# Kernel optimization log

Hardware: AMD Instinct MI355X
Metric: run time of the kernel (lower is better)

## Reference

```python
import jax, jax.numpy as jnp
import numpy as np

N_NODES = 100000
N_EDGES = 1600000
D_IN = 128
D_HID = 128
N_CLASSES = 8


def setup_inputs() -> dict:
    key = jax.random.key(0)
    ks = jax.random.split(key, 8)
    x = jax.random.normal(ks[0], (N_NODES, D_IN), dtype=jnp.float32)
    edge_index = jax.random.randint(ks[1], (2, N_EDGES), 0, N_NODES, dtype=jnp.int32)
    # Glorot-ish init for weights, zeros for biases (PyG GCNConv default)
    W1 = jax.random.normal(ks[2], (D_IN, D_HID), dtype=jnp.float32) / np.sqrt(D_IN)
    b1 = jnp.zeros((D_HID,), dtype=jnp.float32)
    W2 = jax.random.normal(ks[3], (D_HID, D_HID), dtype=jnp.float32) / np.sqrt(D_HID)
    b2 = jnp.zeros((D_HID,), dtype=jnp.float32)
    Wout = jax.random.normal(ks[4], (D_HID, N_CLASSES), dtype=jnp.float32) / np.sqrt(D_HID)
    bout = jnp.zeros((N_CLASSES,), dtype=jnp.float32)
    return {"x": x, "edge_index": edge_index, "W1": W1, "b1": b1,
            "W2": W2, "b2": b2, "Wout": Wout, "bout": bout}


def _gcn_conv(h, src, dst, norm, W, b, n_nodes):
    # h: [N, d_in]; src/dst: [E+N] (with self-loops); norm: [E+N]
    h = h @ W                                   # [N, d_out]
    msg = h[src] * norm[:, None]                # gather + edge-wise scale
    agg = jax.ops.segment_sum(msg, dst, num_segments=n_nodes)  # scatter-add
    return agg + b


def reference(x, edge_index, W1, b1, W2, b2, Wout, bout):
    n = x.shape[0]
    loops = jnp.arange(n, dtype=edge_index.dtype)
    src = jnp.concatenate([edge_index[0], loops])   # [E+N]
    dst = jnp.concatenate([edge_index[1], loops])   # [E+N]
    # symmetric normalization D^-1/2 (A+I) D^-1/2
    deg = jax.ops.segment_sum(jnp.ones_like(src, dtype=x.dtype), dst, num_segments=n)
    dinv = jnp.where(deg > 0, jax.lax.rsqrt(deg), 0.0)
    norm = dinv[src] * dinv[dst]                    # [E+N]

    h = _gcn_conv(x, src, dst, norm, W1, b1, n)
    h = jax.nn.relu(h)  # dropout is identity in eval mode
    h = _gcn_conv(h, src, dst, norm, W2, b2, n)
    h = jax.nn.relu(h)
    return jax.nn.softmax(h @ Wout + bout, axis=1)  # [N, 8]
```

## Files before the change

### kernel.cpp

```cpp
#include <hip/hip_runtime.h>
#include <hip/hip_fp16.h>

#define NN 100000
#define NE 1600000
#define D 128
#define NC 8
#define NBUCK 391
#define BCAP 6144
#define CHUNK 4096
#define NBLK_SC ((NE + CHUNK - 1) / CHUNK)

typedef _Float16 half8 __attribute__((ext_vector_type(8)));
typedef float f32x4 __attribute__((ext_vector_type(4)));

__global__ __launch_bounds__(256) void k_scat(const int* __restrict__ src,
                                              const int* __restrict__ dst,
                                              int* __restrict__ bcursor,
                                              int* __restrict__ staged,
                                              const float* __restrict__ W1,
                                              __half* __restrict__ wt1,
                                              const float* __restrict__ W2,
                                              __half* __restrict__ wt2, int E) {
    const int t = threadIdx.x;
    if (blockIdx.x >= NBLK_SC) {
        const float* W = (blockIdx.x - NBLK_SC) ? W2 : W1;
        __half* wt = (blockIdx.x - NBLK_SC) ? wt2 : wt1;
        for (int i = t; i < D * D; i += 256) {
            int k = i >> 7, c = i & 127;
            wt[c * D + k] = __float2half(W[i]);
        }
        return;
    }
    __shared__ int h[NBUCK];
    __shared__ int cur[NBUCK];
    for (int i = t; i < NBUCK; i += 256) h[i] = 0;
    __syncthreads();
    const int base0 = blockIdx.x * CHUNK;
    int4 d4[4], s4[4];
    bool val[4];
#pragma unroll
    for (int i = 0; i < 4; ++i) {
        int e = base0 + i * 1024 + t * 4;
        val[i] = e < E;
        if (val[i]) {
            d4[i] = *(const int4*)&dst[e];
            s4[i] = *(const int4*)&src[e];
            atomicAdd(&h[d4[i].x >> 8], 1);
            atomicAdd(&h[d4[i].y >> 8], 1);
            atomicAdd(&h[d4[i].z >> 8], 1);
            atomicAdd(&h[d4[i].w >> 8], 1);
        }
    }
    __syncthreads();
    for (int i = t; i < NBUCK; i += 256) {
        int c = h[i];
        cur[i] = c ? (i * BCAP + atomicAdd(&bcursor[i], c)) : 0;
    }
    __syncthreads();
#pragma unroll
    for (int i = 0; i < 4; ++i) {
        if (val[i]) {
            int p;
            p = atomicAdd(&cur[d4[i].x >> 8], 1); staged[p] = s4[i].x * 256 + (d4[i].x & 255);
            p = atomicAdd(&cur[d4[i].y >> 8], 1); staged[p] = s4[i].y * 256 + (d4[i].y & 255);
            p = atomicAdd(&cur[d4[i].z >> 8], 1); staged[p] = s4[i].z * 256 + (d4[i].z & 255);
            p = atomicAdd(&cur[d4[i].w >> 8], 1); staged[p] = s4[i].w * 256 + (d4[i].w & 255);
        }
    }
}

template <bool F32IN, bool SCALE>
__device__ __forceinline__ void gemm_body(const void* __restrict__ Ain,
                                          const __half* __restrict__ wt,
                                          const float* __restrict__ dinv,
                                          __half* __restrict__ hout, int gb) {
    const int tid = threadIdx.x;
    const int lane = tid & 63;
    const int wave = tid >> 6;
    const int wr = wave >> 1, wc = wave & 1;
    const int row0 = gb * 32 + wr * 16;
    const int arow = row0 + (lane & 15);
    const int kg = lane >> 4;

    half8 afrag[4];
    if constexpr (F32IN) {
        const float* A = (const float*)Ain;
#pragma unroll
        for (int s = 0; s < 4; ++s) {
            const float* p = &A[(size_t)arow * D + s * 32 + kg * 8];
            float4 f0 = *(const float4*)p;
            float4 f1 = *(const float4*)(p + 4);
            half8 a;
            a[0] = (_Float16)f0.x; a[1] = (_Float16)f0.y;
            a[2] = (_Float16)f0.z; a[3] = (_Float16)f0.w;
            a[4] = (_Float16)f1.x; a[5] = (_Float16)f1.y;
            a[6] = (_Float16)f1.z; a[7] = (_Float16)f1.w;
            afrag[s] = a;
        }
    } else {
        const __half* A = (const __half*)Ain;
#pragma unroll
        for (int s = 0; s < 4; ++s)
            afrag[s] = *(const half8*)&A[(size_t)arow * D + s * 32 + kg * 8];
    }

    f32x4 acc[4] = {};
    const int colbase = wc * 64;
#pragma unroll
    for (int c = 0; c < 4; ++c) {
        const int col = colbase + c * 16 + (lane & 15);
#pragma unroll
        for (int s = 0; s < 4; ++s) {
            half8 b = *(const half8*)&wt[col * D + s * 32 + kg * 8];
            acc[c] = __builtin_amdgcn_mfma_f32_16x16x32_f16(afrag[s], b, acc[c], 0, 0, 0);
        }
    }

#pragma unroll
    for (int r = 0; r < 4; ++r) {
        const int row = row0 + kg * 4 + r;
        float dv = 1.0f;
        if constexpr (SCALE) dv = dinv[row];
#pragma unroll
        for (int c = 0; c < 4; ++c) {
            const int col = colbase + c * 16 + (lane & 15);
            hout[(size_t)row * D + col] = __float2half(SCALE ? acc[c][r] * dv : acc[c][r]);
        }
    }
}

__global__ __launch_bounds__(256) void k_fg(const int* __restrict__ staged,
                                            const int* __restrict__ bcursor,
                                            int* __restrict__ rowstart,
                                            int* __restrict__ cnt,
                                            float* __restrict__ dinv,
                                            int* __restrict__ csr,
                                            const float* __restrict__ x,
                                            const __half* __restrict__ wt1,
                                            __half* __restrict__ hout) {
    const int b = blockIdx.x;
    if (b >= NBUCK) {
        gemm_body<true, false>(x, wt1, nullptr, hout, b - NBUCK);
        return;
    }
    const int t = threadIdx.x;
    const int bs = b * BCAP;
    const int be = bs + bcursor[b];
    __shared__ int lc[256];
    __shared__ int ls[256];
    __shared__ int sd[256];
    lc[t] = 0;
    __syncthreads();
    for (int i = bs + t; i < be; i += 256) {
        atomicAdd(&lc[staged[i] & 255], 1);
    }
    __syncthreads();
    int v = lc[t];
    sd[t] = v;
    __syncthreads();
    for (int off = 1; off < 256; off <<= 1) {
        int y = (t >= off) ? sd[t - off] : 0;
        __syncthreads();
        sd[t] += y;
        __syncthreads();
    }
    int ex = sd[t] - v;
    ls[t] = bs + ex;
    int node = (b << 8) + t;
    if (node < NN) {
        rowstart[node] = bs + ex;
        cnt[node] = v;
        dinv[node] = rsqrtf((float)(v + 1));
    }
    lc[t] = 0;
    __syncthreads();
    for (int i = bs + t; i < be; i += 256) {
        int e = staged[i];
        int li = e & 255;
        int p = atomicAdd(&lc[li], 1);
        csr[ls[li] + p] = e >> 8;
    }
}

__global__ __launch_bounds__(256) void k_gemm2(const __half* __restrict__ A,
                                               const __half* __restrict__ wt,
                                               const float* __restrict__ dinv,
                                               __half* __restrict__ hout) {
    gemm_body<false, true>(A, wt, dinv, hout, blockIdx.x);
}

__device__ inline void add8h(float* acc, float4 raw) {
    const __half2* hp = (const __half2*)&raw;
#pragma unroll
    for (int q = 0; q < 4; ++q) {
        float2 f = __half22float2(hp[q]);
        acc[2 * q] += f.x;
        acc[2 * q + 1] += f.y;
    }
}

__device__ inline void fma8h(float* acc, float4 raw, float s) {
    const __half2* hp = (const __half2*)&raw;
#pragma unroll
    for (int q = 0; q < 4; ++q) {
        float2 f = __half22float2(hp[q]);
        acc[2 * q] = fmaf(s, f.x, acc[2 * q]);
        acc[2 * q + 1] = fmaf(s, f.y, acc[2 * q + 1]);
    }
}

__global__ __launch_bounds__(256) void k_agg_u(const __half* __restrict__ hs,
                                               const int* __restrict__ rowstart,
                                               const int* __restrict__ cnt,
                                               const int* __restrict__ csr_src,
                                               const float* __restrict__ dinv,
                                               const float* __restrict__ bias,
                                               __half* __restrict__ hout) {
    const int node = blockIdx.x * 4 + (threadIdx.x >> 6);
    const int lane = threadIdx.x & 63;
    const int g = lane >> 4;
    const int f8 = (lane & 15) << 3;

    const float dvn = dinv[node];
    float acc[8] = {};
    if (g == 0) fma8h(acc, *(const float4*)&hs[(size_t)node * D + f8], dvn);

    const int c = cnt[node];
    const int* __restrict__ cl = csr_src + rowstart[node];

    int t = g;
    while (t < c) {
        float4 v[8];
        float dv8[8];
#pragma unroll
        for (int i = 0; i < 8; ++i) {
            int tt = t + 4 * i;
            if (tt < c) {
                int s = cl[tt];
                v[i] = *(const float4*)&hs[(size_t)s * D + f8];
                dv8[i] = dinv[s];
            }
        }
#pragma unroll
        for (int i = 0; i < 8; ++i) {
            int tt = t + 4 * i;
            if (tt < c) fma8h(acc, v[i], dv8[i]);
        }
        t += 32;
    }

#pragma unroll
    for (int q = 0; q < 8; ++q) {
        acc[q] += __shfl_xor(acc[q], 16);
        acc[q] += __shfl_xor(acc[q], 32);
    }

    if (g == 0) {
        float r[8];
#pragma unroll
        for (int q = 0; q < 8; ++q) r[q] = fmaxf(fmaf(dvn, acc[q], bias[f8 + q]), 0.f);
        union { float4 f; __half2 h[4]; } u;
#pragma unroll
        for (int q = 0; q < 4; ++q) u.h[q] = __floats2half2_rn(r[2 * q], r[2 * q + 1]);
        *(float4*)&hout[(size_t)node * D + f8] = u.f;
    }
}

__global__ __launch_bounds__(256) void k_agg_s(const __half* __restrict__ hs,
                                               const int* __restrict__ rowstart,
                                               const int* __restrict__ cnt,
                                               const int* __restrict__ csr_src,
                                               const float* __restrict__ dinv,
                                               const float* __restrict__ bias,
                                               __half* __restrict__ hout) {
    const int node = blockIdx.x * 4 + (threadIdx.x >> 6);
    const int lane = threadIdx.x & 63;
    const int g = lane >> 4;
    const int f8 = (lane & 15) << 3;

    float acc[8] = {};
    if (g == 0) add8h(acc, *(const float4*)&hs[(size_t)node * D + f8]);

    const int c = cnt[node];
    const int* __restrict__ cl = csr_src + rowstart[node];

    int t = g;
    while (t < c) {
        float4 v[8];
#pragma unroll
        for (int i = 0; i < 8; ++i) {
            int tt = t + 4 * i;
            if (tt < c) {
                int s = cl[tt];
                v[i] = *(const float4*)&hs[(size_t)s * D + f8];
            }
        }
#pragma unroll
        for (int i = 0; i < 8; ++i) {
            int tt = t + 4 * i;
            if (tt < c) add8h(acc, v[i]);
        }
        t += 32;
    }

#pragma unroll
    for (int q = 0; q < 8; ++q) {
        acc[q] += __shfl_xor(acc[q], 16);
        acc[q] += __shfl_xor(acc[q], 32);
    }

    if (g == 0) {
        const float dv = dinv[node];
        float r[8];
#pragma unroll
        for (int q = 0; q < 8; ++q) r[q] = fmaxf(fmaf(dv, acc[q], bias[f8 + q]), 0.f);
        union { float4 f; __half2 h[4]; } u;
#pragma unroll
        for (int q = 0; q < 4; ++q) u.h[q] = __floats2half2_rn(r[2 * q], r[2 * q + 1]);
        *(float4*)&hout[(size_t)node * D + f8] = u.f;
    }
}

__global__ void k_out(const __half* __restrict__ h, const float* __restrict__ Wout,
                      const float* __restrict__ bout, float* __restrict__ out, int n) {
    __shared__ float ws[D * NC];
    int tid = threadIdx.x;
    for (int i = tid; i < D * NC; i += 256) ws[i] = Wout[i];
    __syncthreads();
    int node = blockIdx.x * 32 + (tid >> 3);
    int c = tid & 7;
    if (node >= n) return;
    float acc = bout[c];
    const __half* hrow = &h[(size_t)node * D];
#pragma unroll
    for (int k8 = 0; k8 < 16; ++k8) {
        float4 raw = *(const float4*)&hrow[k8 * 8];
        const __half2* hp = (const __half2*)&raw;
#pragma unroll
        for (int q = 0; q < 4; ++q) {
            float2 f = __half22float2(hp[q]);
            int k = k8 * 8 + 2 * q;
            acc += f.x * ws[k * NC + c] + f.y * ws[(k + 1) * NC + c];
        }
    }
    float m = acc;
#pragma unroll
    for (int off = 1; off < 8; off <<= 1) m = fmaxf(m, __shfl_xor(m, off));
    float e = __expf(acc - m);
    float ssum = e;
#pragma unroll
    for (int off = 1; off < 8; off <<= 1) ssum += __shfl_xor(ssum, off);
    out[(size_t)node * NC + c] = e / ssum;
}

extern "C" void kernel_launch(void* const* d_in, const int* in_sizes, int n_in,
                              void* d_out, int out_size, void* d_ws, size_t ws_size,
                              hipStream_t stream) {
    const float* x    = (const float*)d_in[0];
    const int*   ei   = (const int*)d_in[1];
    const float* W1   = (const float*)d_in[2];
    const float* b1   = (const float*)d_in[3];
    const float* W2   = (const float*)d_in[4];
    const float* b2   = (const float*)d_in[5];
    const float* Wout = (const float*)d_in[6];
    const float* bout = (const float*)d_in[7];
    float* out = (float*)d_out;

    size_t off = 0;
    char* base = (char*)d_ws;
    auto alloc = [&](size_t bytes) -> void* {
        void* p = base + off;
        off += (bytes + 255) & ~(size_t)255;
        return p;
    };
    int*    cnt      = (int*)alloc((size_t)NN * 4);
    int*    rowstart = (int*)alloc((size_t)NN * 4);
    int*    bcursor  = (int*)alloc((size_t)NBUCK * 4);
    int*    csr      = (int*)alloc((size_t)NBUCK * BCAP * 4);
    float*  dinv     = (float*)alloc((size_t)NN * 4);
    __half* wt1      = (__half*)alloc((size_t)D * D * 2);
    __half* wt2      = (__half*)alloc((size_t)D * D * 2);
    __half* h16a     = (__half*)alloc((size_t)NN * D * 2);
    __half* h16f     = (__half*)alloc((size_t)NN * D * 2);
    __half* h16b     = (__half*)alloc((size_t)NN * D * 2);
    int*    staged   = (int*)alloc((size_t)NBUCK * BCAP * 4);
    if (off > ws_size) return;

    const int* src = ei;
    const int* dst = ei + NE;

    hipMemsetAsync(bcursor, 0, (size_t)NBUCK * 4, stream);

    k_scat<<<NBLK_SC + 2, 256, 0, stream>>>(src, dst, bcursor, staged,
                                            W1, wt1, W2, wt2, NE);

    k_fg<<<NBUCK + NN / 32, 256, 0, stream>>>(staged, bcursor, rowstart, cnt, dinv,
                                              csr, x, wt1, h16a);

    int agg_grid = NN / 4;
    k_agg_u<<<agg_grid, 256, 0, stream>>>(h16a, rowstart, cnt, csr, dinv, b1, h16f);
    k_gemm2<<<NN / 32, 256, 0, stream>>>(h16f, wt2, dinv, h16a);
    k_agg_s<<<agg_grid, 256, 0, stream>>>(h16a, rowstart, cnt, csr, dinv, b2, h16b);
    k_out<<<(NN + 31) / 32, 256, 0, stream>>>(h16b, Wout, bout, out, NN);
}
```

Measured before the change: 269.9 us.

## Fuse layer-1 aggregation with layer-2 GEMM and prescale GEMM1 output by dinv

Splits the old fused CSR-fill plus GEMM1 kernel into a separate bucket-fill kernel followed by GEMM1. GEMM1 now needs dinv, so it prescales rows by dinv and the layer-1 aggregation no longer has to load dinv[src] per edge. The layer-1 aggregation is fused with the layer-2 GEMM: each block aggregates 16 nodes into shared memory and multiplies them by W2 with MFMA. This removes one kernel and one full fp16 intermediate write and read. In exchange, GEMM1 can no longer overlap with the CSR build, and the fused kernel has a barrier and fewer waves per node.

```diff
diff --git a/kernel.cpp b/kernel.cpp
--- a/kernel.cpp
+++ b/kernel.cpp
@@ -69,80 +69,13 @@
     }
 }
 
-template <bool F32IN, bool SCALE>
-__device__ __forceinline__ void gemm_body(const void* __restrict__ Ain,
-                                          const __half* __restrict__ wt,
-                                          const float* __restrict__ dinv,
-                                          __half* __restrict__ hout, int gb) {
-    const int tid = threadIdx.x;
-    const int lane = tid & 63;
-    const int wave = tid >> 6;
-    const int wr = wave >> 1, wc = wave & 1;
-    const int row0 = gb * 32 + wr * 16;
-    const int arow = row0 + (lane & 15);
-    const int kg = lane >> 4;
-
-    half8 afrag[4];
-    if constexpr (F32IN) {
-        const float* A = (const float*)Ain;
-#pragma unroll
-        for (int s = 0; s < 4; ++s) {
-            const float* p = &A[(size_t)arow * D + s * 32 + kg * 8];
-            float4 f0 = *(const float4*)p;
-            float4 f1 = *(const float4*)(p + 4);
-            half8 a;
-            a[0] = (_Float16)f0.x; a[1] = (_Float16)f0.y;
-            a[2] = (_Float16)f0.z; a[3] = (_Float16)f0.w;
-            a[4] = (_Float16)f1.x; a[5] = (_Float16)f1.y;
-            a[6] = (_Float16)f1.z; a[7] = (_Float16)f1.w;
-            afrag[s] = a;
-        }
-    } else {
-        const __half* A = (const __half*)Ain;
-#pragma unroll
-        for (int s = 0; s < 4; ++s)
-            afrag[s] = *(const half8*)&A[(size_t)arow * D + s * 32 + kg * 8];
-    }
-
-    f32x4 acc[4] = {};
-    const int colbase = wc * 64;
-#pragma unroll
-    for (int c = 0; c < 4; ++c) {
-        const int col = colbase + c * 16 + (lane & 15);
-#pragma unroll
-        for (int s = 0; s < 4; ++s) {
-            half8 b = *(const half8*)&wt[col * D + s * 32 + kg * 8];
-            acc[c] = __builtin_amdgcn_mfma_f32_16x16x32_f16(afrag[s], b, acc[c], 0, 0, 0);
-        }
-    }
-
-#pragma unroll
-    for (int r = 0; r < 4; ++r) {
-        const int row = row0 + kg * 4 + r;
-        float dv = 1.0f;
-        if constexpr (SCALE) dv = dinv[row];
-#pragma unroll
-        for (int c = 0; c < 4; ++c) {
-            const int col = colbase + c * 16 + (lane & 15);
-            hout[(size_t)row * D + col] = __float2half(SCALE ? acc[c][r] * dv : acc[c][r]);
-        }
-    }
-}
-
-__global__ __launch_bounds__(256) void k_fg(const int* __restrict__ staged,
-                                            const int* __restrict__ bcursor,
-                                            int* __restrict__ rowstart,
-                                            int* __restrict__ cnt,
-                                            float* __restrict__ dinv,
-                                            int* __restrict__ csr,
-                                            const float* __restrict__ x,
-                                            const __half* __restrict__ wt1,
-                                            __half* __restrict__ hout) {
+__global__ __launch_bounds__(256) void k_bfill(const int* __restrict__ staged,
+                                               const int* __restrict__ bcursor,
+                                               int* __restrict__ rowstart,
+                                               int* __restrict__ cnt,
+                                               float* __restrict__ dinv,
+                                               int* __restrict__ csr) {
     const int b = blockIdx.x;
-    if (b >= NBUCK) {
-        gemm_body<true, false>(x, wt1, nullptr, hout, b - NBUCK);
-        return;
-    }
     const int t = threadIdx.x;
     const int bs = b * BCAP;
     const int be = bs + bcursor[b];
@@ -182,11 +115,54 @@
     }
 }
 
-__global__ __launch_bounds__(256) void k_gemm2(const __half* __restrict__ A,
+__global__ __launch_bounds__(256) void k_gemm1(const float* __restrict__ A,
                                                const __half* __restrict__ wt,
                                                const float* __restrict__ dinv,
                                                __half* __restrict__ hout) {
-    gemm_body<false, true>(A, wt, dinv, hout, blockIdx.x);
+    const int tid = threadIdx.x;
+    const int lane = tid & 63;
+    const int wave = tid >> 6;
+    const int wr = wave >> 1, wc = wave & 1;
+    const int row0 = blockIdx.x * 32 + wr * 16;
+    const int arow = row0 + (lane & 15);
+    const int kg = lane >> 4;
+
+    half8 afrag[4];
+#pragma unroll
+    for (int s = 0; s < 4; ++s) {
+        const float* p = &A[(size_t)arow * D + s * 32 + kg * 8];
+        float4 f0 = *(const float4*)p;
+        float4 f1 = *(const float4*)(p + 4);
+        half8 a;
+        a[0] = (_Float16)f0.x; a[1] = (_Float16)f0.y;
+        a[2] = (_Float16)f0.z; a[3] = (_Float16)f0.w;
+        a[4] = (_Float16)f1.x; a[5] = (_Float16)f1.y;
+        a[6] = (_Float16)f1.z; a[7] = (_Float16)f1.w;
+        afrag[s] = a;
+    }
+
+    f32x4 acc[4] = {};
+    const int colbase = wc * 64;
+#pragma unroll
+    for (int c = 0; c < 4; ++c) {
+        const int col = colbase + c * 16 + (lane & 15);
+#pragma unroll
+        for (int s = 0; s < 4; ++s) {
+            half8 b = *(const half8*)&wt[col * D + s * 32 + kg * 8];
+            acc[c] = __builtin_amdgcn_mfma_f32_16x16x32_f16(afrag[s], b, acc[c], 0, 0, 0);
+        }
+    }
+
+#pragma unroll
+    for (int r = 0; r < 4; ++r) {
+        const int row = row0 + kg * 4 + r;
+        const float dv = dinv[row];
+#pragma unroll
+        for (int c = 0; c < 4; ++c) {
+            const int col = colbase + c * 16 + (lane & 15);
+            hout[(size_t)row * D + col] = __float2half(acc[c][r] * dv);
+        }
+    }
 }
 
 __device__ inline void add8h(float* acc, float4 raw) {
@@ -199,80 +175,96 @@
     }
 }
 
-__device__ inline void fma8h(float* acc, float4 raw, float s) {
-    const __half2* hp = (const __half2*)&raw;
-#pragma unroll
-    for (int q = 0; q < 4; ++q) {
-        float2 f = __half22float2(hp[q]);
-        acc[2 * q] = fmaf(s, f.x, acc[2 * q]);
-        acc[2 * q + 1] = fmaf(s, f.y, acc[2 * q + 1]);
-    }
-}
-
-__global__ __launch_bounds__(256) void k_agg_u(const __half* __restrict__ hs,
-                                               const int* __restrict__ rowstart,
-                                               const int* __restrict__ cnt,
-                                               const int* __restrict__ csr_src,
-                                               const float* __restrict__ dinv,
-                                               const float* __restrict__ bias,
-                                               __half* __restrict__ hout) {
-    const int node = blockIdx.x * 4 + (threadIdx.x >> 6);
+__global__ __launch_bounds__(256) void k_aggemm(const __half* __restrict__ hs,
+                                                const int* __restrict__ rowstart,
+                                                const int* __restrict__ cnt,
+                                                const int* __restrict__ csr_src,
+                                                const float* __restrict__ dinv,
+                                                const float* __restrict__ b1,
+                                                const __half* __restrict__ wt2,
+                                                __half* __restrict__ hout) {
+    __shared__ __align__(16) __half rows[16][136];
+    const int w = threadIdx.x >> 6;
     const int lane = threadIdx.x & 63;
     const int g = lane >> 4;
     const int f8 = (lane & 15) << 3;
-
-    const float dvn = dinv[node];
-    float acc[8] = {};
-    if (g == 0) fma8h(acc, *(const float4*)&hs[(size_t)node * D + f8], dvn);
-
-    const int c = cnt[node];
-    const int* __restrict__ cl = csr_src + rowstart[node];
-
-    int t = g;
-    while (t < c) {
-        float4 v[8];
-        float dv8[8];
-#pragma unroll
-        for (int i = 0; i < 8; ++i) {
-            int tt = t + 4 * i;
-            if (tt < c) {
-                int s = cl[tt];
-                v[i] = *(const float4*)&hs[(size_t)s * D + f8];
-                dv8[i] = dinv[s];
+    const int nb = blockIdx.x * 16;
+
+    for (int k = 0; k < 4; ++k) {
+        const int node = nb + w * 4 + k;
+        float acc[8] = {};
+        if (g == 0) add8h(acc, *(const float4*)&hs[(size_t)node * D + f8]);
+        const int c = cnt[node];
+        const int* __restrict__ cl = csr_src + rowstart[node];
+        int t = g;
+        while (t < c) {
+            float4 v[8];
+#pragma unroll
+            for (int i = 0; i < 8; ++i) {
+                int tt = t + 4 * i;
+                if (tt < c) v[i] = *(const float4*)&hs[(size_t)cl[tt] * D + f8];
             }
-        }
-#pragma unroll
-        for (int i = 0; i < 8; ++i) {
-            int tt = t + 4 * i;
-            if (tt < c) fma8h(acc, v[i], dv8[i]);
-        }
-        t += 32;
-    }
-
-#pragma unroll
-    for (int q = 0; q < 8; ++q) {
-        acc[q] += __shfl_xor(acc[q], 16);
-        acc[q] += __shfl_xor(acc[q], 32);
-    }
-
-    if (g == 0) {
-        float r[8];
-#pragma unroll
-        for (int q = 0; q < 8; ++q) r[q] = fmaxf(fmaf(dvn, acc[q], bias[f8 + q]), 0.f);
-        union { float4 f; __half2 h[4]; } u;
-#pragma unroll
-        for (int q = 0; q < 4; ++q) u.h[q] = __floats2half2_rn(r[2 * q], r[2 * q + 1]);
-        *(float4*)&hout[(size_t)node * D + f8] = u.f;
-    }
-}
-
-__global__ __launch_bounds__(256) void k_agg_s(const __half* __restrict__ hs,
-                                               const int* __restrict__ rowstart,
-                                               const int* __restrict__ cnt,
-                                               const int* __restrict__ csr_src,
-                                               const float* __restrict__ dinv,
-                                               const float* __restrict__ bias,
-                                               __half* __restrict__ hout) {
+#pragma unroll
+            for (int i = 0; i < 8; ++i) {
+                int tt = t + 4 * i;
+                if (tt < c) add8h(acc, v[i]);
+            }
+            t += 32;
+        }
+#pragma unroll
+        for (int q = 0; q < 8; ++q) {
+            acc[q] += __shfl_xor(acc[q], 16);
+            acc[q] += __shfl_xor(acc[q], 32);
+        }
+        if (g == 0) {
+            const float dv = dinv[node];
+            union { float4 f; __half2 h2[4]; } u;
+#pragma unroll
+            for (int q = 0; q < 4; ++q) {
+                float r0 = fmaxf(fmaf(dv, acc[2 * q], b1[f8 + 2 * q]), 0.f);
+                float r1 = fmaxf(fmaf(dv, acc[2 * q + 1], b1[f8 + 2 * q + 1]), 0.f);
+                u.h2[q] = __floats2half2_rn(r0, r1);
+            }
+            *(float4*)&rows[w * 4 + k][f8] = u.f;
+        }
+    }
+    __syncthreads();
+
+    const int kg = lane >> 4;
+    const int l15 = lane & 15;
+    half8 afrag[4];
+#pragma unroll
+    for (int s = 0; s < 4; ++s)
+        afrag[s] = *(const half8*)&rows[l15][s * 32 + kg * 8];
+    f32x4 acc2[2] = {};
+#pragma unroll
+    for (int ct = 0; ct < 2; ++ct) {
+        const int col = w * 32 + ct * 16 + l15;
+#pragma unroll
+        for (int s = 0; s < 4; ++s) {
+            half8 b = *(const half8*)&wt2[col * D + s * 32 + kg * 8];
+            acc2[ct] = __builtin_amdgcn_mfma_f32_16x16x32_f16(afrag[s], b, acc2[ct], 0, 0, 0);
+        }
+    }
+#pragma unroll
+    for (int r = 0; r < 4; ++r) {
+        const int row = nb + kg * 4 + r;
+        const float dv = dinv[row];
+#pragma unroll
+        for (int ct = 0; ct < 2; ++ct) {
+            const int col = w * 32 + ct * 16 + l15;
+            hout[(size_t)row * D + col] = __float2half(acc2[ct][r] * dv);
+        }
+    }
+}
+
+__global__ __launch_bounds__(256) void k_agg(const __half* __restrict__ hs,
+                                             const int* __restrict__ rowstart,
+                                             const int* __restrict__ cnt,
+                                             const int* __restrict__ csr_src,
+                                             const float* __restrict__ dinv,
+                                             const float* __restrict__ bias,
+                                             __half* __restrict__ hout) {
     const int node = blockIdx.x * 4 + (threadIdx.x >> 6);
     const int lane = threadIdx.x & 63;
     const int g = lane >> 4;
@@ -381,7 +373,7 @@
     __half* wt1      = (__half*)alloc((size_t)D * D * 2);
     __half* wt2      = (__half*)alloc((size_t)D * D * 2);
     __half* h16a     = (__half*)alloc((size_t)NN * D * 2);
-    __half* h16f     = (__half*)alloc((size_t)NN * D * 2);
+    __half* h16g     = (__half*)alloc((size_t)NN * D * 2);
     __half* h16b     = (__half*)alloc((size_t)NN * D * 2);
     int*    staged   = (int*)alloc((size_t)NBUCK * BCAP * 4);
     if (off > ws_size) return;
@@ -393,13 +385,11 @@
 
     k_scat<<<NBLK_SC + 2, 256, 0, stream>>>(src, dst, bcursor, staged,
                                             W1, wt1, W2, wt2, NE);
-
-    k_fg<<<NBUCK + NN / 32, 256, 0, stream>>>(staged, bcursor, rowstart, cnt, dinv,
-                                              csr, x, wt1, h16a);
-
-    int agg_grid = NN / 4;
-    k_agg_u<<<agg_grid, 256, 0, stream>>>(h16a, rowstart, cnt, csr, dinv, b1, h16f);
-    k_gemm2<<<NN / 32, 256, 0, stream>>>(h16f, wt2, dinv, h16a);
-    k_agg_s<<<agg_grid, 256, 0, stream>>>(h16a, rowstart, cnt, csr, dinv, b2, h16b);
+    k_bfill<<<NBUCK, 256, 0, stream>>>(staged, bcursor, rowstart, cnt, dinv, csr);
+
+    k_gemm1<<<NN / 32, 256, 0, stream>>>(x, wt1, dinv, h16a);
+    k_aggemm<<<NN / 16, 256, 0, stream>>>(h16a, rowstart, cnt, csr, dinv, b1,
+                                          wt2, h16g);
+    k_agg<<<NN / 4, 256, 0, stream>>>(h16g, rowstart, cnt, csr, dinv, b2, h16b);
     k_out<<<(NN + 31) / 32, 256, 0, stream>>>(h16b, Wout, bout, out, NN);
 }
```

After: 272.3 us. No clear change (+0.9%).
